# Kernel tuning notes

Hardware: AMD Instinct MI355X
Metric: run time of the kernel (lower is better)

Reference implementation:

```python
import jax, jax.numpy as jnp
import numpy as np

B, I, C, K, L = 4, 4, 256, 7, 5
SIZES = [160, 80, 40, 20, 10]


def setup_inputs() -> dict:
    key = jax.random.key(0)
    ks = jax.random.split(key, 10)
    inp = {}
    for i, s in enumerate(SIZES):
        inp[f"feats_x{i}"] = jax.random.normal(ks[i], (B, C, s, s), jnp.float32)
    inp["modulator"] = jax.random.normal(ks[5], (B, I, C, K, K), jnp.float32)
    # conv weights ~ normal_init(std=0.01), biases zero
    inp["pm_w"] = 0.01 * jax.random.normal(ks[6], (L, C, C, K, K), jnp.float32)
    inp["pm_b"] = jnp.zeros((L, C), jnp.float32)
    inp["po_w"] = 0.01 * jax.random.normal(ks[7], (L, C, C), jnp.float32)
    inp["po_b"] = jnp.zeros((L, C), jnp.float32)
    return inp


def reference(feats_x0, feats_x1, feats_x2, feats_x3, feats_x4,
              modulator, pm_w, pm_b, po_w, po_b):
    """Batched version of RPN_Modulator.inference: for every (image i, instance j,
    level k): q = Conv7x7(modulator[i,j]) -> [C,1,1]; out = Conv1x1(q * feats_x[k][i]).
    Vectorized over images and instances instead of nested Python loops."""
    feats = [feats_x0, feats_x1, feats_x2, feats_x3, feats_x4]
    outs = []
    for k in range(L):
        # 7x7 valid conv on a 7x7 crop == full contraction -> per-instance channel vector
        q = jnp.einsum('bichw,ochw->bio', modulator, pm_w[k]) + pm_b[k]  # [B,I,C]
        # channel-wise modulation of the gallery feature map
        m = q[:, :, :, None, None] * feats[k][:, None]                   # [B,I,C,H,W]
        # 1x1 output projection
        o = jnp.einsum('bichw,oc->biohw', m, po_w[k]) \
            + po_b[k][None, None, :, None, None]                          # [B,I,C,H,W]
        outs.append(o)
    return tuple(outs)
```

## Files before the change

### kernel.cpp

```cpp
#include <hip/hip_runtime.h>
#include <hip/hip_bf16.h>


typedef __bf16 bf16x8 __attribute__((ext_vector_type(8)));
typedef float  f32x4  __attribute__((ext_vector_type(4)));
typedef unsigned short u16;

__device__ __forceinline__ unsigned pack2(float lo, float hi) {
    __hip_bfloat162 h = __float22bfloat162_rn(make_float2(lo, hi));
    union { __hip_bfloat162 h; unsigned u; } cv; cv.h = h; return cv.u;
}

__device__ __forceinline__ void decode_tile(int x, int& k, int& nt, int& N, size_t& oo) {
    if (x < 400)      { k = 0; nt = x;       N = 25600; oo = 0; }
    else if (x < 500) { k = 1; nt = x - 400; N = 6400;  oo = 104857600; }
    else if (x < 525) { k = 2; nt = x - 500; N = 1600;  oo = 131072000; }
    else if (x < 532) { k = 3; nt = x - 525; N = 400;   oo = 137625600; }
    else              { k = 4; nt = x - 532; N = 100;   oo = 139264000; }
}

__global__ __launch_bounds__(256) void k_q(
    const float* __restrict__ modulator,
    const float* __restrict__ pm_w,
    float* __restrict__ qpart)
{
    int o2 = blockIdx.x;
    int k  = blockIdx.y;
    int s  = blockIdx.z;
    int t  = threadIdx.x;
    float accA[16], accB[16];
#pragma unroll
    for (int i = 0; i < 16; ++i) { accA[i] = 0.f; accB[i] = 0.f; }
    const float4* mod4 = (const float4*)modulator;
    const float4* wa4  = (const float4*)(pm_w + ((size_t)k * 256 + o2) * 12544);
    const float4* wb4  = (const float4*)(pm_w + ((size_t)k * 256 + o2 + 128) * 12544);
    for (int it = 0; it < 4; ++it) {
        int jj = it * 256 + t;
        if (jj < 784) {
            int j = s * 784 + jj;
            float4 wa = wa4[j], wb = wb4[j];
#pragma unroll
            for (int bi = 0; bi < 16; ++bi) {
                float4 m = mod4[bi * 3136 + j];
                accA[bi] += wa.x * m.x + wa.y * m.y + wa.z * m.z + wa.w * m.w;
                accB[bi] += wb.x * m.x + wb.y * m.y + wb.z * m.z + wb.w * m.w;
            }
        }
    }
#pragma unroll
    for (int bi = 0; bi < 16; ++bi) {
#pragma unroll
        for (int off = 32; off > 0; off >>= 1) {
            accA[bi] += __shfl_down(accA[bi], off);
            accB[bi] += __shfl_down(accB[bi], off);
        }
    }
    __shared__ float red[4][32];
    int w = t >> 6, lane = t & 63;
    if (lane == 0) {
#pragma unroll
        for (int bi = 0; bi < 16; ++bi) { red[w][bi] = accA[bi]; red[w][16 + bi] = accB[bi]; }
    }
    __syncthreads();
    if (t < 32) {
        float v = red[0][t] + red[1][t] + red[2][t] + red[3][t];
        int bi = t & 15;
        int o  = (t < 16) ? o2 : (o2 + 128);
        qpart[(((size_t)s * 5 + k) * 16 + bi) * 256 + o] = v;
    }
}

__global__ __launch_bounds__(256) void k_w2(
    const float* __restrict__ po_w,
    const float* __restrict__ pm_b,
    const float* __restrict__ qpart,
    u16* __restrict__ w2)
{
    int idx4 = blockIdx.x * 256 + threadIdx.x;
    int c4 = idx4 & 63;
    int o  = (idx4 >> 6) & 255;
    int bi = (idx4 >> 14) & 15;
    int k  = idx4 >> 18;
    size_t qi = ((size_t)(k * 16 + bi)) * 256 + c4 * 4;
    f32x4 q0 = *(const f32x4*)(qpart + qi);
    f32x4 q1 = *(const f32x4*)(qpart + qi + 20480);
    f32x4 q2 = *(const f32x4*)(qpart + qi + 40960);
    f32x4 q3 = *(const f32x4*)(qpart + qi + 61440);
    f32x4 pb = *(const f32x4*)(pm_b + k * 256 + c4 * 4);
    f32x4 q  = q0 + q1 + q2 + q3 + pb;
    f32x4 w  = *(const f32x4*)(po_w + ((size_t)(k * 256 + o)) * 256 + c4 * 4);
    uint2 r;
    r.x = pack2(w[0] * q[0], w[1] * q[1]);
    r.y = pack2(w[2] * q[2], w[3] * q[3]);
    *(uint2*)(w2 + (size_t)idx4 * 4) = r;
}

__global__ __launch_bounds__(512, 4) void k_gemm(
    const float* __restrict__ f0, const float* __restrict__ f1,
    const float* __restrict__ f2, const float* __restrict__ f3,
    const float* __restrict__ f4,
    const u16* __restrict__ w2,
    const float* __restrict__ po_b,
    float* __restrict__ out)
{
    __shared__ __align__(16) u16 ldsB[64 * 256];
    int k, nt, N; size_t oo;
    decode_tile(blockIdx.x, k, nt, N, oo);
    const float* fsrc = (k == 0) ? f0 : (k == 1) ? f1 : (k == 2) ? f2 : (k == 3) ? f3 : f4;
    const int b = blockIdx.y;
    const int t = threadIdx.x;
    const int n0 = nt * 64;

    {
        const float* s = fsrc + (size_t)b * 256 * N + n0;
        int ng = t & 15, grp = t >> 4;
        bool inb = (n0 + ng * 4) < N;
#pragma unroll
        for (int j = 0; j < 4; ++j) {
            int p = j * 32 + grp;
            f32x4 v0 = {0.f, 0.f, 0.f, 0.f}, v1 = {0.f, 0.f, 0.f, 0.f};
            if (inb) {
                v0 = *(const f32x4*)(s + (size_t)(2 * p) * N + ng * 4);
                v1 = *(const f32x4*)(s + (size_t)(2 * p + 1) * N + ng * 4);
            }
#pragma unroll
            for (int e = 0; e < 4; ++e) {
                int n = ng * 4 + e;
                unsigned off = (unsigned)(n << 9) + (unsigned)(p << 2);
                off ^= (unsigned)((n & 7) << 4);
                *(unsigned*)((char*)ldsB + off) = pack2(v0[e], v1[e]);
            }
        }
    }
    __syncthreads();

    const int lane = t & 63, w = t >> 6;
    const int lr = lane & 15, lg = lane >> 4;
    const float* pb = po_b + k * 256;
    float* obase0 = out + oo;

#pragma unroll 1
    for (int i = 0; i < 4; ++i) {
        const u16* wsrc = w2 + ((size_t)(k * 16 + b * 4 + i) << 16);
        float* obase = obase0 + (size_t)(b * 4 + i) * 256 * N;
        f32x4 acc[2][4];
#pragma unroll
        for (int mi = 0; mi < 2; ++mi)
#pragma unroll
            for (int ni = 0; ni < 4; ++ni)
                acc[mi][ni] = (f32x4){0.f, 0.f, 0.f, 0.f};

#pragma unroll 4
        for (int kk = 0; kk < 8; ++kk) {
            bf16x8 a[2], bb[4];
#pragma unroll
            for (int mi = 0; mi < 2; ++mi)
                a[mi] = *(const bf16x8*)(wsrc + (size_t)(w * 32 + mi * 16 + lr) * 256 + kk * 32 + lg * 8);
#pragma unroll
            for (int ni = 0; ni < 4; ++ni) {
                int row = ni * 16 + lr;
                unsigned off = (unsigned)(row << 9) + (unsigned)(kk << 6) + (unsigned)(lg << 4);
                off ^= (unsigned)((row & 7) << 4);
                bb[ni] = *(const bf16x8*)((const char*)ldsB + off);
            }
#pragma unroll
            for (int mi = 0; mi < 2; ++mi)
#pragma unroll
                for (int ni = 0; ni < 4; ++ni)
                    acc[mi][ni] = __builtin_amdgcn_mfma_f32_16x16x32_bf16(a[mi], bb[ni], acc[mi][ni], 0, 0, 0);
        }

#pragma unroll
        for (int mi = 0; mi < 2; ++mi) {
#pragma unroll
            for (int rr = 0; rr < 4; ++rr) {
                int orow = w * 32 + mi * 16 + lg * 4 + rr;
                float bias = pb[orow];
#pragma unroll
                for (int ni = 0; ni < 4; ++ni) {
                    int ocol = n0 + ni * 16 + lr;
                    if (ocol < N)
                        __builtin_nontemporal_store(acc[mi][ni][rr] + bias,
                                                    obase + (size_t)orow * N + ocol);
                }
            }
        }
    }
}

extern "C" void kernel_launch(void* const* d_in, const int* in_sizes, int n_in,
                              void* d_out, int out_size, void* d_ws, size_t ws_size,
                              hipStream_t stream) {
    const float* f0 = (const float*)d_in[0];
    const float* f1 = (const float*)d_in[1];
    const float* f2 = (const float*)d_in[2];
    const float* f3 = (const float*)d_in[3];
    const float* f4 = (const float*)d_in[4];
    const float* modulator = (const float*)d_in[5];
    const float* pm_w = (const float*)d_in[6];
    const float* pm_b = (const float*)d_in[7];
    const float* po_w = (const float*)d_in[8];
    const float* po_b = (const float*)d_in[9];
    float* out = (float*)d_out;

    u16* w2 = (u16*)d_ws;
    float* qpart = (float*)(w2 + (size_t)5 * 16 * 256 * 256);

    k_q<<<dim3(128, 5, 4), 256, 0, stream>>>(modulator, pm_w, qpart);
    k_w2<<<5120, 256, 0, stream>>>(po_w, pm_b, qpart, w2);
    k_gemm<<<dim3(534, 4), 512, 0, stream>>>(f0, f1, f2, f3, f4, w2, po_b, out);
}
```

Measured before the change: 218.1 us.

## Swap MFMA operand roles for vectorized output stores and widen q-kernel output tiling

The GEMM kernel now feeds the LDS-resident feature tile as the A operand and the global weight matrix as the B operand, with warps split over 4 output-channel groups and 2 spatial groups. Each lane then holds four consecutive spatial outputs, so results go out as 16-byte nontemporal stores instead of scalar stores, and the bias load is hoisted out of the loop. The q kernel computes four output channels per block instead of two, which halves its grid and reuses each modulator load across more weights. The risks are that vector stores need N to be a multiple of 4 (true for all level sizes) and that the q kernel uses more registers.

```diff
diff --git a/kernel.cpp b/kernel.cpp
--- a/kernel.cpp
+++ b/kernel.cpp
@@ -24,48 +24,55 @@
     const float* __restrict__ pm_w,
     float* __restrict__ qpart)
 {
-    int o2 = blockIdx.x;
+    int o4 = blockIdx.x;
     int k  = blockIdx.y;
     int s  = blockIdx.z;
     int t  = threadIdx.x;
-    float accA[16], accB[16];
-#pragma unroll
-    for (int i = 0; i < 16; ++i) { accA[i] = 0.f; accB[i] = 0.f; }
+    float acc[4][16];
+#pragma unroll
+    for (int j = 0; j < 4; ++j)
+#pragma unroll
+        for (int bi = 0; bi < 16; ++bi) acc[j][bi] = 0.f;
     const float4* mod4 = (const float4*)modulator;
-    const float4* wa4  = (const float4*)(pm_w + ((size_t)k * 256 + o2) * 12544);
-    const float4* wb4  = (const float4*)(pm_w + ((size_t)k * 256 + o2 + 128) * 12544);
+    const float4* wp0 = (const float4*)(pm_w + ((size_t)k * 256 + o4      ) * 12544);
+    const float4* wp1 = (const float4*)(pm_w + ((size_t)k * 256 + o4 +  64) * 12544);
+    const float4* wp2 = (const float4*)(pm_w + ((size_t)k * 256 + o4 + 128) * 12544);
+    const float4* wp3 = (const float4*)(pm_w + ((size_t)k * 256 + o4 + 192) * 12544);
     for (int it = 0; it < 4; ++it) {
         int jj = it * 256 + t;
         if (jj < 784) {
-            int j = s * 784 + jj;
-            float4 wa = wa4[j], wb = wb4[j];
+            int jx = s * 784 + jj;
+            float4 wv0 = wp0[jx], wv1 = wp1[jx], wv2 = wp2[jx], wv3 = wp3[jx];
 #pragma unroll
             for (int bi = 0; bi < 16; ++bi) {
-                float4 m = mod4[bi * 3136 + j];
-                accA[bi] += wa.x * m.x + wa.y * m.y + wa.z * m.z + wa.w * m.w;
-                accB[bi] += wb.x * m.x + wb.y * m.y + wb.z * m.z + wb.w * m.w;
-            }
-        }
-    }
-#pragma unroll
-    for (int bi = 0; bi < 16; ++bi) {
-#pragma unroll
-        for (int off = 32; off > 0; off >>= 1) {
-            accA[bi] += __shfl_down(accA[bi], off);
-            accB[bi] += __shfl_down(accB[bi], off);
-        }
-    }
-    __shared__ float red[4][32];
+                float4 m = mod4[bi * 3136 + jx];
+                acc[0][bi] += wv0.x * m.x + wv0.y * m.y + wv0.z * m.z + wv0.w * m.w;
+                acc[1][bi] += wv1.x * m.x + wv1.y * m.y + wv1.z * m.z + wv1.w * m.w;
+                acc[2][bi] += wv2.x * m.x + wv2.y * m.y + wv2.z * m.z + wv2.w * m.w;
+                acc[3][bi] += wv3.x * m.x + wv3.y * m.y + wv3.z * m.z + wv3.w * m.w;
+            }
+        }
+    }
+#pragma unroll
+    for (int j = 0; j < 4; ++j)
+#pragma unroll
+        for (int bi = 0; bi < 16; ++bi)
+#pragma unroll
+            for (int off = 32; off > 0; off >>= 1)
+                acc[j][bi] += __shfl_down(acc[j][bi], off);
+    __shared__ float red[4][64];
     int w = t >> 6, lane = t & 63;
     if (lane == 0) {
 #pragma unroll
-        for (int bi = 0; bi < 16; ++bi) { red[w][bi] = accA[bi]; red[w][16 + bi] = accB[bi]; }
+        for (int j = 0; j < 4; ++j)
+#pragma unroll
+            for (int bi = 0; bi < 16; ++bi) red[w][j * 16 + bi] = acc[j][bi];
     }
     __syncthreads();
-    if (t < 32) {
+    if (t < 64) {
         float v = red[0][t] + red[1][t] + red[2][t] + red[3][t];
         int bi = t & 15;
-        int o  = (t < 16) ? o2 : (o2 + 128);
+        int o  = o4 + (t >> 4) * 64;
         qpart[(((size_t)s * 5 + k) * 16 + bi) * 256 + o] = v;
     }
 }
@@ -136,12 +143,27 @@
 
     const int lane = t & 63, w = t >> 6;
     const int lr = lane & 15, lg = lane >> 4;
+    const int wo = w & 3, wn = w >> 2;
     const float* pb = po_b + k * 256;
     float* obase0 = out + oo;
 
+    unsigned abase[2];
+#pragma unroll
+    for (int mi = 0; mi < 2; ++mi) {
+        int row = wn * 32 + mi * 16 + lr;
+        unsigned off = (unsigned)(row << 9) + (unsigned)(lg << 4);
+        off ^= (unsigned)((row & 7) << 4);
+        abase[mi] = off;
+    }
+
+    float bias[4];
+#pragma unroll
+    for (int ni = 0; ni < 4; ++ni) bias[ni] = pb[wo * 64 + ni * 16 + lr];
+
 #pragma unroll 1
     for (int i = 0; i < 4; ++i) {
-        const u16* wsrc = w2 + ((size_t)(k * 16 + b * 4 + i) << 16);
+        const u16* wsrc = w2 + ((size_t)(k * 16 + b * 4 + i) << 16)
+                        + (size_t)(wo * 64 + lr) * 256 + lg * 8;
         float* obase = obase0 + (size_t)(b * 4 + i) * 256 * N;
         f32x4 acc[2][4];
 #pragma unroll
@@ -152,36 +174,30 @@
 
 #pragma unroll 4
         for (int kk = 0; kk < 8; ++kk) {
-            bf16x8 a[2], bb[4];
+            bf16x8 a[2], bw[4];
 #pragma unroll
             for (int mi = 0; mi < 2; ++mi)
-                a[mi] = *(const bf16x8*)(wsrc + (size_t)(w * 32 + mi * 16 + lr) * 256 + kk * 32 + lg * 8);
-#pragma unroll
-            for (int ni = 0; ni < 4; ++ni) {
-                int row = ni * 16 + lr;
-                unsigned off = (unsigned)(row << 9) + (unsigned)(kk << 6) + (unsigned)(lg << 4);
-                off ^= (unsigned)((row & 7) << 4);
-                bb[ni] = *(const bf16x8*)((const char*)ldsB + off);
-            }
+                a[mi] = *(const bf16x8*)((const char*)ldsB + (abase[mi] ^ (unsigned)(kk << 6)));
+#pragma unroll
+            for (int ni = 0; ni < 4; ++ni)
+                bw[ni] = *(const bf16x8*)(wsrc + ni * 4096 + kk * 32);
 #pragma unroll
             for (int mi = 0; mi < 2; ++mi)
 #pragma unroll
                 for (int ni = 0; ni < 4; ++ni)
-                    acc[mi][ni] = __builtin_amdgcn_mfma_f32_16x16x32_bf16(a[mi], bb[ni], acc[mi][ni], 0, 0, 0);
+                    acc[mi][ni] = __builtin_amdgcn_mfma_f32_16x16x32_bf16(a[mi], bw[ni], acc[mi][ni], 0, 0, 0);
         }
 
 #pragma unroll
         for (int mi = 0; mi < 2; ++mi) {
-#pragma unroll
-            for (int rr = 0; rr < 4; ++rr) {
-                int orow = w * 32 + mi * 16 + lg * 4 + rr;
-                float bias = pb[orow];
+            int nbase = n0 + wn * 32 + mi * 16 + lg * 4;
+            if (nbase < N) {
 #pragma unroll
                 for (int ni = 0; ni < 4; ++ni) {
-                    int ocol = n0 + ni * 16 + lr;
-                    if (ocol < N)
-                        __builtin_nontemporal_store(acc[mi][ni][rr] + bias,
-                                                    obase + (size_t)orow * N + ocol);
+                    int orow = wo * 64 + ni * 16 + lr;
+                    f32x4 v = acc[mi][ni];
+                    v[0] += bias[ni]; v[1] += bias[ni]; v[2] += bias[ni]; v[3] += bias[ni];
+                    __builtin_nontemporal_store(v, (f32x4*)(obase + (size_t)orow * N + nbase));
                 }
             }
         }
@@ -206,7 +222,7 @@
     u16* w2 = (u16*)d_ws;
     float* qpart = (float*)(w2 + (size_t)5 * 16 * 256 * 256);
 
-    k_q<<<dim3(128, 5, 4), 256, 0, stream>>>(modulator, pm_w, qpart);
+    k_q<<<dim3(64, 5, 4), 256, 0, stream>>>(modulator, pm_w, qpart);
     k_w2<<<5120, 256, 0, stream>>>(po_w, pm_b, qpart, w2);
     k_gemm<<<dim3(534, 4), 512, 0, stream>>>(f0, f1, f2, f3, f4, w2, po_b, out);
 }
```

New measurement: 350.2 us. +60.6%, slower.
